# Optimization experiments

Hardware: AMD Instinct MI355X
Metric: run time of the kernel (lower is better)

## Reference

```python
import jax, jax.numpy as jnp
import numpy as np
import math

B, S, D, H = 2, 2048, 1024, 16
D_K = D // H


def setup_inputs() -> dict:
    key = jax.random.key(0)
    ks = jax.random.split(key, 9)
    scale = 0.02
    return {
        "query": jax.random.normal(ks[0], (B, S, D), dtype=jnp.float32),
        "key": jax.random.normal(ks[1], (B, S, D), dtype=jnp.float32),
        "value": jax.random.normal(ks[2], (B, S, D), dtype=jnp.float32),
        "padding_mask": jax.random.bernoulli(ks[3], 0.1, (B, 1, 1, S)),
        "Wq": jax.random.normal(ks[4], (D, D), dtype=jnp.float32) * scale,
        "bq": jnp.zeros((D,), dtype=jnp.float32),
        "Wk": jax.random.normal(ks[5], (D, D), dtype=jnp.float32) * scale,
        "bk": jnp.zeros((D,), dtype=jnp.float32),
        "Wv": jax.random.normal(ks[6], (D, D), dtype=jnp.float32) * scale,
        "bv": jnp.zeros((D,), dtype=jnp.float32),
        "Wo": jax.random.normal(ks[7], (D, D), dtype=jnp.float32) * scale,
        "bo": jnp.zeros((D,), dtype=jnp.float32),
    }


def reference(query, key, value, padding_mask, Wq, bq, Wk, bk, Wv, bv, Wo, bo):
    # projections -> [B, H, S, d_k]
    q = (query @ Wq + bq).reshape(B, S, H, D_K).transpose(0, 2, 1, 3)
    k = (key @ Wk + bk).reshape(B, S, H, D_K).transpose(0, 2, 1, 3)
    v = (value @ Wv + bv).reshape(B, S, H, D_K).transpose(0, 2, 1, 3)

    # scores: [B, H, S, S]
    scores = jnp.einsum("bhqd,bhkd->bhqk", q, k) / math.sqrt(D_K)

    # faithful to original: triu(scores, 1).bool() -> True where upper-tri score != 0,
    # masked positions get value 1e-10 (NOT -inf) before softmax
    causal_mask = jnp.triu(scores, k=1) != 0
    scores = jnp.where(causal_mask, jnp.float32(1e-10), scores)
    scores = jnp.where(padding_mask, jnp.float32(1e-10), scores)

    attn = jax.nn.softmax(scores, axis=-1)
    out = jnp.einsum("bhqk,bhkd->bhqd", attn, v)  # [B, H, S, d_k]
    out = out.transpose(0, 2, 1, 3).reshape(B, S, D)
    return out @ Wo + bo
```

## Files before the change

### kernel.cpp

```cpp
#include <hip/hip_runtime.h>
#include <hip/hip_bf16.h>
#include <cstdint>
#include <cstddef>

typedef __hip_bfloat16 bf16;
typedef __attribute__((ext_vector_type(8))) short short8;
typedef __attribute__((ext_vector_type(4))) short s4v;
typedef __attribute__((ext_vector_type(4))) float floatx4;

#define B_ 2
#define S_ 2048
#define D_ 1024
#define H_ 16
#define DK_ 64
#define M_ 4096
#define HEADELEMS 131072
#define TILEELEMS 4096
#define QSCALE 0.1803368801111204f

struct __align__(8) bf16x4 { bf16 x, y, z, w; };

__device__ __forceinline__ floatx4 mfma16(short8 a, short8 b, floatx4 c) {
  return __builtin_amdgcn_mfma_f32_16x16x32_bf16(a, b, c, 0, 0, 0);
}
__device__ __forceinline__ void gl_lds16(const bf16* g, bf16* l) {
  __builtin_amdgcn_global_load_lds((const __attribute__((address_space(1))) void*)g,
                                   (__attribute__((address_space(3))) void*)l, 16, 0, 0);
}
__device__ __forceinline__ float bs2f(short s) {
  bf16 b = *reinterpret_cast<bf16*>(&s);
  return __bfloat162float(b);
}
__device__ __forceinline__ s4v pack4(float p0, float p1, float p2, float p3) {
  union { __hip_bfloat162 h; short2 s; } ua, ub;
  ua.h = __float22bfloat162_rn(make_float2(p0, p1));
  ub.h = __float22bfloat162_rn(make_float2(p2, p3));
  s4v r = {ua.s.x, ua.s.y, ub.s.x, ub.s.y};
  return r;
}
__device__ __forceinline__ float fast_exp2(float x) {
#if __has_builtin(__builtin_amdgcn_exp2f)
  return __builtin_amdgcn_exp2f(x);
#else
  float r; asm("v_exp_f32 %0, %1" : "=v"(r) : "v"(x)); return r;
#endif
}

__global__ void prep_kernel(const float* __restrict__ q_in, const float* __restrict__ k_in,
                            const float* __restrict__ v_in,
                            const float* __restrict__ Wq, const float* __restrict__ Wk,
                            const float* __restrict__ Wv, const float* __restrict__ Wo,
                            bf16* __restrict__ xq, bf16* __restrict__ xk, bf16* __restrict__ xv,
                            bf16* __restrict__ wqt, bf16* __restrict__ wkt,
                            bf16* __restrict__ wvt, bf16* __restrict__ wot,
                            const unsigned int* __restrict__ pmask, int* __restrict__ flag) {
  __shared__ bf16 tile[64][66];
  __shared__ int sbyte;
  const int blk = blockIdx.x;
  const int tid = threadIdx.x;
  if (blk < 12288) {
    const int z = blk >> 12;
    const int i = ((blk & 4095) << 8) | tid;
    const float* src = (z == 0) ? q_in : (z == 1) ? k_in : v_in;
    bf16* dst = (z == 0) ? xq : (z == 1) ? xk : xv;
    float4 v = ((const float4*)src)[i];
    bf16x4 o = { __float2bfloat16(v.x), __float2bfloat16(v.y),
                 __float2bfloat16(v.z), __float2bfloat16(v.w) };
    ((bf16x4*)dst)[i] = o;
  } else if (blk < 13312) {
    const int t = blk - 12288;
    const int z = t >> 8;
    const int rc = t & 255;
    const int r0 = (rc >> 4) * 64, c0 = (rc & 15) * 64;
    const float* src = (z == 0) ? Wq : (z == 1) ? Wk : (z == 2) ? Wv : Wo;
    bf16* dst = (z == 0) ? wqt : (z == 1) ? wkt : (z == 2) ? wvt : wot;
    const int lr = tid >> 4;
    const int lc4 = (tid & 15) * 4;
#pragma unroll
    for (int i = 0; i < 4; ++i) {
      const int r = lr + i * 16;
      float4 v = *(const float4*)(src + (size_t)(r0 + r) * D_ + c0 + lc4);
      tile[r][lc4 + 0] = __float2bfloat16(v.x);
      tile[r][lc4 + 1] = __float2bfloat16(v.y);
      tile[r][lc4 + 2] = __float2bfloat16(v.z);
      tile[r][lc4 + 3] = __float2bfloat16(v.w);
    }
    __syncthreads();
    const int orr = tid & 63;
    const int oc0 = tid >> 6;
#pragma unroll
    for (int j = 0; j < 16; ++j) {
      const int oc = oc0 + j * 4;
      dst[(size_t)(c0 + oc) * D_ + r0 + orr] = tile[orr][oc];
    }
  } else {
    if (tid == 0) sbyte = 0;
    __syncthreads();
    for (int i = tid; i < (B_ * S_) / 4; i += 256) {
      const unsigned int v = pmask[i];
      if (((v & 0xFEFEFEFEu) == 0u) && ((v & 0xFFFFFF00u) != 0u)) sbyte = 1;
    }
    __syncthreads();
    if (tid == 0) *flag = sbyte;
  }
}

template<int MT>
__global__ __launch_bounds__(256, 2) void gemm_k(
    const bf16* __restrict__ A0, const bf16* __restrict__ A1, const bf16* __restrict__ A2,
    const bf16* __restrict__ W0, const bf16* __restrict__ W1, const bf16* __restrict__ W2,
    const float* __restrict__ b0, const float* __restrict__ b1, const float* __restrict__ b2,
    void* __restrict__ O0, void* __restrict__ O1, void* __restrict__ O2,
    const int mode01, const int Kd, const float sc)
{
  constexpr int ROWS = MT + 128;
  __shared__ __align__(16) bf16 sh[2 * ROWS * 64];
  const int z = blockIdx.z;
  const bf16* A = (z == 0) ? A0 : (z == 1) ? A1 : A2;
  const bf16* W = (z == 0) ? W0 : (z == 1) ? W1 : W2;
  const float* bias = (z == 0) ? b0 : (z == 1) ? b1 : b2;
  void* Cout = (z == 0) ? O0 : (z == 1) ? O1 : O2;
  const int mode = (z == 2) ? 1 : mode01;
  const float scz = (z == 0) ? sc : 1.f;

  constexpr int MI = MT / 32;
  const int tid = threadIdx.x;
  const int wave = tid >> 6, lane = tid & 63;
  const int quad = lane >> 4, lc = lane & 15;
  const int wm = (wave >> 1) * (MT / 2), wn = (wave & 1) * 64;
  const int m0 = blockIdx.x * MT, n0 = blockIdx.y * 128;

  const floatx4 zero4 = {0.f, 0.f, 0.f, 0.f};
  floatx4 acc[MI][4];
#pragma unroll
  for (int mi = 0; mi < MI; ++mi)
#pragma unroll
    for (int ni = 0; ni < 4; ++ni) acc[mi][ni] = zero4;

  const int srow = lane >> 3;
  const int schunk = ((lane & 7) ^ srow) * 8;
  const bf16* Ag = A + (size_t)(m0 + wave * (MT / 4) + srow) * Kd + schunk;
  const bf16* Bg = W + (size_t)(n0 + wave * 32 + srow) * Kd + schunk;

  auto stage = [&](bf16* buf, int k0) {
    bf16* As0 = buf + wave * (MT / 4) * 64;
    bf16* Bs0 = buf + MT * 64 + wave * 32 * 64;
#pragma unroll
    for (int j = 0; j < MT / 32; ++j)
      gl_lds16(Ag + k0 + (size_t)(j * 8) * Kd, As0 + j * 512);
#pragma unroll
    for (int j = 0; j < 4; ++j)
      gl_lds16(Bg + k0 + (size_t)(j * 8) * Kd, Bs0 + j * 512);
  };

  stage(sh, 0);
  asm volatile("s_waitcnt vmcnt(0)" ::: "memory");
  __syncthreads();

  int cur = 0;
  for (int k0 = 0; k0 < Kd; k0 += 64) {
    bf16* cbuf = cur ? sh + ROWS * 64 : sh;
    bf16* nbuf = cur ? sh : sh + ROWS * 64;
    const bool more = (k0 + 64 < Kd);
    if (more) stage(nbuf, k0 + 64);

    const bf16* Ar = cbuf;
    const bf16* Br = cbuf + MT * 64;
    short8 af[2][MI], bfr[2][4];
#pragma unroll
    for (int kk = 0; kk < 2; ++kk) {
#pragma unroll
      for (int i = 0; i < MI; ++i)
        af[kk][i] = *(const short8*)(Ar + (wm + i * 16 + lc) * 64
                                     + (((kk * 4 + quad) ^ (lc & 7)) * 8));
#pragma unroll
      for (int i = 0; i < 4; ++i)
        bfr[kk][i] = *(const short8*)(Br + (wn + i * 16 + lc) * 64
                                      + (((kk * 4 + quad) ^ (lc & 7)) * 8));
    }
#pragma unroll
    for (int kk = 0; kk < 2; ++kk)
#pragma unroll
      for (int mi = 0; mi < MI; ++mi)
#pragma unroll
        for (int ni = 0; ni < 4; ++ni)
          acc[mi][ni] = mfma16(af[kk][mi], bfr[kk][ni], acc[mi][ni]);

    __syncthreads();
    cur ^= 1;
  }

  if (mode == 2) {
    float* out = (float*)Cout;
#pragma unroll
    for (int mi = 0; mi < MI; ++mi)
#pragma unroll
      for (int ni = 0; ni < 4; ++ni) {
        const int col = n0 + wn + ni * 16 + lc;
        const float bv = bias[col];
        const int rbase = m0 + wm + mi * 16 + quad * 4;
#pragma unroll
        for (int r = 0; r < 4; ++r)
          out[(size_t)(rbase + r) * D_ + col] = acc[mi][ni][r] + bv;
      }
  } else {
    bf16* pool = sh + wave * 2048;
    float bvs[4];
#pragma unroll
    for (int ni = 0; ni < 4; ++ni) bvs[ni] = bias[n0 + wn + ni * 16 + lc];
    const int hcol = (n0 + wn) >> 6;
    const int mglob = m0 + wm;
    bf16* outb = (bf16*)Cout + (size_t)((mglob >> 11) * H_ + hcol) * HEADELEMS
               + (size_t)((mglob & (S_ - 1)) >> 6) * TILEELEMS;
#pragma unroll
    for (int half = 0; half < MI / 2; ++half) {
#pragma unroll
      for (int mi2 = 0; mi2 < 2; ++mi2) {
        const int mi = half * 2 + mi2;
#pragma unroll
        for (int ni = 0; ni < 4; ++ni) {
          const int dkl = ni * 16 + lc;
#pragma unroll
          for (int r = 0; r < 4; ++r) {
            const float v = (acc[mi][ni][r] + bvs[ni]) * scz;
            int idx;
            if (mode == 0) {
              const int c = (mi2 * 2 + (dkl >> 5)) * 64 + ((dkl >> 3) & 3) * 16 + quad * 4 + r;
              idx = c * 8 + (dkl & 7);
            } else {
              const int c = (mi2 * 4 + (dkl >> 4)) * 64 + quad * 16 + (dkl & 15);
              idx = c * 4 + r;
            }
            pool[idx] = __float2bfloat16(v);
          }
        }
      }
#pragma unroll
      for (int t = 0; t < 4; ++t) {
        const short8 vv = *(const short8*)(pool + t * 512 + lane * 8);
        *(short8*)(outb + half * 2048 + t * 512 + lane * 8) = vv;
      }
    }
  }
}

__global__ void suf_kernel(const bf16* __restrict__ vp, float* __restrict__ suf) {
  __shared__ float ts[32 * 64];
  const int bhid = blockIdx.x;
  const bf16* vb = vp + (size_t)bhid * HEADELEMS;
  const int tid = threadIdx.x;
  const int dk = tid & 63, g = tid >> 6;
  const int dkt = dk >> 4, lck = dk & 15;
  for (int T = g * 8; T < g * 8 + 8; ++T) {
    float sum = 0.f;
#pragma unroll
    for (int w = 0; w < 4; ++w)
#pragma unroll
      for (int qd = 0; qd < 4; ++qd) {
        const s4v x = *(const s4v*)(vb + (size_t)T * TILEELEMS
                                    + (size_t)(((w * 4 + dkt) * 64 + qd * 16 + lck)) * 4);
        sum += bs2f(x[0]) + bs2f(x[1]) + bs2f(x[2]) + bs2f(x[3]);
      }
    ts[T * 64 + dk] = sum;
  }
  __syncthreads();
  if (g == 0) {
    float run = 0.f;
    float* out = suf + (size_t)bhid * (33 * 64);
    out[32 * 64 + dk] = 0.f;
    for (int T = 31; T >= 0; --T) { run += ts[T * 64 + dk]; out[T * 64 + dk] = run; }
  }
}

template<bool DIAGP>
__device__ __forceinline__ void qk_tile(const short8 ak0, const short8 ak1,
                                        const short8 (&qf)[4][2],
                                        const unsigned int (&pmb)[4], const int T,
                                        short8 (&pB)[4], const int half,
                                        const int w, const int quad, const int lc,
                                        const bool diag) {
  const floatx4 z4 = {0.f, 0.f, 0.f, 0.f};
  const short ONE = (short)0x3F80;
  bool mm[4];
#pragma unroll
  for (int r = 0; r < 4; ++r) mm[r] = ((pmb[r] >> T) & 1u) != 0u;
#pragma unroll
  for (int qt = 0; qt < 4; ++qt) {
    if (DIAGP && diag && w > qt) {
      s4v o1 = {ONE, ONE, ONE, ONE};
      ((s4v*)&pB[qt])[half] = o1;
      continue;
    }
    floatx4 s = mfma16(ak0, qf[qt][0], z4);
    s = mfma16(ak1, qf[qt][1], s);
    float pv[4];
#pragma unroll
    for (int r = 0; r < 4; ++r) {
      bool m = mm[r];
      if (DIAGP && diag && w == qt) m = m || (quad * 4 + r > lc);
      pv[r] = m ? 1.f : fast_exp2(s[r]);
    }
    ((s4v*)&pB[qt])[half] = pack4(pv[0], pv[1], pv[2], pv[3]);
  }
}

__device__ __forceinline__ void pv_step(const short8 (&av)[4], const short8 (&pB)[4],
                                        const short8 ones, floatx4 (&lsum)[4],
                                        floatx4 (&oacc)[4][4]) {
#pragma unroll
  for (int qt = 0; qt < 4; ++qt) lsum[qt] = mfma16(ones, pB[qt], lsum[qt]);
#pragma unroll
  for (int dkt = 0; dkt < 4; ++dkt)
#pragma unroll
    for (int qt = 0; qt < 4; ++qt)
      oacc[dkt][qt] = mfma16(av[dkt], pB[qt], oacc[dkt][qt]);
}

__device__ __forceinline__ void stage8(const bf16* kb, const bf16* vb, bf16* slot,
                                       const int T0, const int T1,
                                       const int wl, const int wreg) {
  const bf16* k0 = kb + (size_t)T0 * TILEELEMS + wl;
  const bf16* k1 = kb + (size_t)T1 * TILEELEMS + wl;
  const bf16* v0 = vb + (size_t)T0 * TILEELEMS + wl;
  const bf16* v1 = vb + (size_t)T1 * TILEELEMS + wl;
  gl_lds16(k0,       slot + wreg);
  gl_lds16(k0 + 512, slot + wreg + 512);
  gl_lds16(k1,       slot + 4096 + wreg);
  gl_lds16(k1 + 512, slot + 4096 + wreg + 512);
  gl_lds16(v0,       slot + 8192 + wreg);
  gl_lds16(v0 + 512, slot + 8192 + wreg + 512);
  gl_lds16(v1,       slot + 12288 + wreg);
  gl_lds16(v1 + 512, slot + 12288 + wreg + 512);
}

__global__ __launch_bounds__(256, 2) void attn_kernel(
    const bf16* __restrict__ qp, const bf16* __restrict__ kp,
    const bf16* __restrict__ vp, const float* __restrict__ suf,
    const void* __restrict__ pad, const int* __restrict__ flag,
    bf16* __restrict__ oa)
{
  __shared__ __align__(16) bf16 lds[32768];

  const int lin = blockIdx.x;
  const int xcd = lin & 7;
  const int t = lin >> 3;
  const int grp = t >> 4;
  const int jq = t & 15;
  const int bh = xcd + 8 * grp;
  const int b = bh >> 4, h = bh & 15;

  const int tid = threadIdx.x;
  const int w = tid >> 6, lane = tid & 63, quad = lane >> 4, lc = lane & 15;
  const int bytemode = *flag;

  const int wreg = w * 1024;
  const int wl = wreg + lane * 8;
  const int vl = wreg + lane * 4;

  const bf16* kb = kp + (size_t)bh * HEADELEMS;
  const bf16* vb = vp + (size_t)bh * HEADELEMS;

  const short ONE = (short)0x3F80;
  const short8 ones = {ONE, ONE, ONE, ONE, ONE, ONE, ONE, ONE};

  unsigned int pmb[4] = {0u, 0u, 0u, 0u};
  if (bytemode) {
    const unsigned char* pp = (const unsigned char*)pad + b * S_ + w * 16 + quad * 4;
#pragma unroll
    for (int T = 0; T < 32; ++T) {
      const uchar4 u = *(const uchar4*)(pp + T * 64);
      pmb[0] |= (u.x ? 1u : 0u) << T;
      pmb[1] |= (u.y ? 1u : 0u) << T;
      pmb[2] |= (u.z ? 1u : 0u) << T;
      pmb[3] |= (u.w ? 1u : 0u) << T;
    }
  } else {
    const int* pp = (const int*)pad + b * S_ + w * 16 + quad * 4;
#pragma unroll
    for (int T = 0; T < 32; ++T) {
      const int4 u = *(const int4*)(pp + (size_t)T * 64);
      pmb[0] |= (u.x ? 1u : 0u) << T;
      pmb[1] |= (u.y ? 1u : 0u) << T;
      pmb[2] |= (u.z ? 1u : 0u) << T;
      pmb[3] |= (u.w ? 1u : 0u) << T;
    }
  }

#pragma unroll 1
  for (int qsel = 0; qsel < 2; ++qsel) {
    const int myqt = qsel ? jq : 31 - jq;
    const int mynt = myqt + 1;
    const int np = (mynt + 1) >> 1;

    const bf16* qb = qp + (size_t)bh * HEADELEMS + (size_t)myqt * TILEELEMS;
    gl_lds16(qb + wl,       lds + 16384 + wreg);
    gl_lds16(qb + wl + 512, lds + 16384 + wreg + 512);
    stage8(kb, vb, lds, 0, 1, wl, wreg);
    asm volatile("s_waitcnt vmcnt(0)" ::: "memory");
    __syncthreads();

    short8 qf[4][2];
#pragma unroll
    for (int qt = 0; qt < 4; ++qt)
#pragma unroll
      for (int hh = 0; hh < 2; ++hh)
        qf[qt][hh] = *(const short8*)(lds + 16384 + qt * 1024 + hh * 512 + lane * 8);
    __syncthreads();

    const floatx4 zero4 = {0.f, 0.f, 0.f, 0.f};
    floatx4 oacc[4][4];
#pragma unroll
    for (int i = 0; i < 4; ++i)
#pragma unroll
      for (int jj = 0; jj < 4; ++jj) oacc[i][jj] = zero4;
    floatx4 lsum[4] = {zero4, zero4, zero4, zero4};

#pragma unroll 1
    for (int p = 0; p < np; ++p) {
      const bool more = (p + 1 < np);
      if (more) {
        stage8(kb, vb, lds + (((p + 1) & 1) << 14), 2 * p + 2, 2 * p + 3, wl, wreg);
        asm volatile("s_waitcnt vmcnt(12)" ::: "memory");
      } else {
        asm volatile("s_waitcnt vmcnt(4)" ::: "memory");
      }
      __builtin_amdgcn_sched_barrier(0);

      bf16* slot = lds + ((p & 1) << 14);
      const short8 ak00 = *(const short8*)(slot + wl);
      const short8 ak01 = *(const short8*)(slot + wl + 512);
      const short8 ak10 = *(const short8*)(slot + 4096 + wl);
      const short8 ak11 = *(const short8*)(slot + 4096 + wl + 512);

      const int T0 = 2 * p, T1 = 2 * p + 1;
      short8 pB[4];
      if (more) {
        qk_tile<false>(ak00, ak01, qf, pmb, T0, pB, 0, w, quad, lc, false);
        qk_tile<false>(ak10, ak11, qf, pmb, T1, pB, 1, w, quad, lc, false);
      } else {
        qk_tile<true>(ak00, ak01, qf, pmb, T0, pB, 0, w, quad, lc, T0 == mynt - 1);
        if (T1 < mynt) {
          qk_tile<true>(ak10, ak11, qf, pmb, T1, pB, 1, w, quad, lc, true);
        } else {
          const s4v zz = {0, 0, 0, 0};
#pragma unroll
          for (int qt = 0; qt < 4; ++qt) ((s4v*)&pB[qt])[1] = zz;
        }
      }

      if (more) asm volatile("s_waitcnt vmcnt(8)" ::: "memory");
      else      asm volatile("s_waitcnt vmcnt(0)" ::: "memory");
      __builtin_amdgcn_sched_barrier(0);

      short8 av[4];
#pragma unroll
      for (int dkt = 0; dkt < 4; ++dkt) {
        ((s4v*)&av[dkt])[0] = *(const s4v*)(slot + 8192 + vl + dkt * 256);
        ((s4v*)&av[dkt])[1] = *(const s4v*)(slot + 12288 + vl + dkt * 256);
      }
      pv_step(av, pB, ones, lsum, oacc);
    }

    __syncthreads();

    float* fbuf = (float*)lds;
    bf16* obuf = lds + 8704;
    float* lbuf = (float*)(lds + 13312);

#pragma unroll
    for (int qt = 0; qt < 4; ++qt)
      if (quad == 0) lbuf[w * 64 + qt * 16 + lc] = lsum[qt][0];
    __syncthreads();
    float ls = lbuf[0 * 64 + w * 16 + lc] + lbuf[1 * 64 + w * 16 + lc]
             + lbuf[2 * 64 + w * 16 + lc] + lbuf[3 * 64 + w * 16 + lc];
    ls += (float)(S_ - mynt * 64);
    const float linv = 1.f / ls;
    const float* sufp = suf + (size_t)bh * (33 * 64) + mynt * 64;

#pragma unroll
    for (int dktG = 0; dktG < 4; ++dktG) {
#pragma unroll
      for (int qt = 0; qt < 4; ++qt) {
        const floatx4 a = oacc[dktG][qt];
        float* dst = fbuf + (w * 4 + qt) * 272 + lc;
#pragma unroll
        for (int r = 0; r < 4; ++r) dst[(quad * 4 + r) * 17] = a[r];
      }
      __syncthreads();
      const float4 sv4 = *(const float4*)(sufp + dktG * 16 + quad * 4);
      float v[4];
#pragma unroll
      for (int r = 0; r < 4; ++r) {
        const int e = (quad * 4 + r) * 17 + lc;
        v[r] = fbuf[(0 * 4 + w) * 272 + e] + fbuf[(1 * 4 + w) * 272 + e]
             + fbuf[(2 * 4 + w) * 272 + e] + fbuf[(3 * 4 + w) * 272 + e];
      }
      v[0] = (v[0] + sv4.x) * linv; v[1] = (v[1] + sv4.y) * linv;
      v[2] = (v[2] + sv4.z) * linv; v[3] = (v[3] + sv4.w) * linv;
      bf16x4 pk = { __float2bfloat16(v[0]), __float2bfloat16(v[1]),
                    __float2bfloat16(v[2]), __float2bfloat16(v[3]) };
      *(bf16x4*)(obuf + (w * 16 + lc) * 72 + dktG * 16 + quad * 4) = pk;
      __syncthreads();
    }

    const size_t obase = (size_t)(b * S_ + myqt * 64) * D_ + h * 64;
#pragma unroll
    for (int it = 0; it < 2; ++it) {
      const int idx = it * 256 + tid;
      const int row = idx >> 3, c8 = (idx & 7) * 8;
      const short8 vv = *(const short8*)(obuf + row * 72 + c8);
      *(short8*)(oa + obase + (size_t)row * D_ + c8) = vv;
    }
    __syncthreads();
  }
}

extern "C" void kernel_launch(void* const* d_in, const int* in_sizes, int n_in,
                              void* d_out, int out_size, void* d_ws, size_t ws_size,
                              hipStream_t stream) {
  (void)in_sizes; (void)n_in; (void)out_size; (void)ws_size;
  const float* q_in = (const float*)d_in[0];
  const float* k_in = (const float*)d_in[1];
  const float* v_in = (const float*)d_in[2];
  const void*  pmask = d_in[3];
  const float* Wq = (const float*)d_in[4];
  const float* bq = (const float*)d_in[5];
  const float* Wk = (const float*)d_in[6];
  const float* bk = (const float*)d_in[7];
  const float* Wv = (const float*)d_in[8];
  const float* bv = (const float*)d_in[9];
  const float* Wo = (const float*)d_in[10];
  const float* bo = (const float*)d_in[11];

  char* ws = (char*)d_ws;
  bf16* xq  = (bf16*)(ws + 0);
  bf16* xk  = (bf16*)(ws + 8388608);
  bf16* xv  = (bf16*)(ws + 16777216);
  bf16* wqt = (bf16*)(ws + 25165824);
  bf16* wkt = (bf16*)(ws + 27262976);
  bf16* wvt = (bf16*)(ws + 29360128);
  bf16* wot = (bf16*)(ws + 31457280);
  bf16* qpp = (bf16*)(ws + 33554432);
  bf16* kpp = (bf16*)(ws + 41943040);
  bf16* vpp = (bf16*)(ws + 50331648);
  float* suf = (float*)(ws + 25165824);
  int*  flg = (int*)(ws + 58720256);
  bf16* oa  = xq;

  prep_kernel<<<13313, 256, 0, stream>>>(q_in, k_in, v_in, Wq, Wk, Wv, Wo,
                                         xq, xk, xv, wqt, wkt, wvt, wot,
                                         (const unsigned int*)pmask, flg);

  gemm_k<128><<<dim3(32, 8, 3), 256, 0, stream>>>(xq, xk, xv, wqt, wkt, wvt,
                                                  bq, bk, bv, qpp, kpp, vpp, 0, D_, QSCALE);
  suf_kernel<<<32, 256, 0, stream>>>(vpp, suf);

  attn_kernel<<<512, 256, 0, stream>>>(qpp, kpp, vpp, suf, pmask, flg, oa);

  gemm_k<128><<<dim3(32, 8, 1), 256, 0, stream>>>(oa, oa, oa, wot, wot, wot,
                                                  bo, bo, bo, d_out, d_out, d_out, 2, D_, 1.f);
}
```

Baseline: 221.4 us.

## Split attention to one query tile per block with single-buffered per-wave LDS

Each attention block now handles a single query tile instead of a balanced pair, so 1024 blocks are launched. A rotated index mapping spreads the short and long causal tiles evenly across blocks. LDS is halved by dropping the double buffer: each wave reads its own K/V slice into registers, then immediately issues the next global-to-LDS loads into the same slots. Together with launch bounds of 4 blocks per CU, the aim is to raise occupancy and let other waves hide load latency. The cost is less prefetch overlap inside a single wave and more per-block prologue and epilogue overhead.

```diff
diff --git a/kernel.cpp b/kernel.cpp
--- a/kernel.cpp
+++ b/kernel.cpp
@@ -19,6 +19,7 @@
 #define QSCALE 0.1803368801111204f
 
 struct __align__(8) bf16x4 { bf16 x, y, z, w; };
+struct __align__(4) bf16x2 { bf16 x, y; };
 
 __device__ __forceinline__ floatx4 mfma16(short8 a, short8 b, floatx4 c) {
   return __builtin_amdgcn_mfma_f32_16x16x32_bf16(a, b, c, 0, 0, 0);
@@ -213,10 +214,10 @@
     bf16* outb = (bf16*)Cout + (size_t)((mglob >> 11) * H_ + hcol) * HEADELEMS
                + (size_t)((mglob & (S_ - 1)) >> 6) * TILEELEMS;
 #pragma unroll
-    for (int half = 0; half < MI / 2; ++half) {
+    for (int half2 = 0; half2 < MI / 2; ++half2) {
 #pragma unroll
       for (int mi2 = 0; mi2 < 2; ++mi2) {
-        const int mi = half * 2 + mi2;
+        const int mi = half2 * 2 + mi2;
 #pragma unroll
         for (int ni = 0; ni < 4; ++ni) {
           const int dkl = ni * 16 + lc;
@@ -238,7 +239,7 @@
 #pragma unroll
       for (int t = 0; t < 4; ++t) {
         const short8 vv = *(const short8*)(pool + t * 512 + lane * 8);
-        *(short8*)(outb + half * 2048 + t * 512 + lane * 8) = vv;
+        *(short8*)(outb + half2 * 2048 + t * 512 + lane * 8) = vv;
       }
     }
   }
@@ -304,50 +305,25 @@
   }
 }
 
-__device__ __forceinline__ void pv_step(const short8 (&av)[4], const short8 (&pB)[4],
-                                        const short8 ones, floatx4 (&lsum)[4],
-                                        floatx4 (&oacc)[4][4]) {
-#pragma unroll
-  for (int qt = 0; qt < 4; ++qt) lsum[qt] = mfma16(ones, pB[qt], lsum[qt]);
-#pragma unroll
-  for (int dkt = 0; dkt < 4; ++dkt)
-#pragma unroll
-    for (int qt = 0; qt < 4; ++qt)
-      oacc[dkt][qt] = mfma16(av[dkt], pB[qt], oacc[dkt][qt]);
-}
-
-__device__ __forceinline__ void stage8(const bf16* kb, const bf16* vb, bf16* slot,
-                                       const int T0, const int T1,
-                                       const int wl, const int wreg) {
-  const bf16* k0 = kb + (size_t)T0 * TILEELEMS + wl;
-  const bf16* k1 = kb + (size_t)T1 * TILEELEMS + wl;
-  const bf16* v0 = vb + (size_t)T0 * TILEELEMS + wl;
-  const bf16* v1 = vb + (size_t)T1 * TILEELEMS + wl;
-  gl_lds16(k0,       slot + wreg);
-  gl_lds16(k0 + 512, slot + wreg + 512);
-  gl_lds16(k1,       slot + 4096 + wreg);
-  gl_lds16(k1 + 512, slot + 4096 + wreg + 512);
-  gl_lds16(v0,       slot + 8192 + wreg);
-  gl_lds16(v0 + 512, slot + 8192 + wreg + 512);
-  gl_lds16(v1,       slot + 12288 + wreg);
-  gl_lds16(v1 + 512, slot + 12288 + wreg + 512);
-}
-
-__global__ __launch_bounds__(256, 2) void attn_kernel(
+__global__ __launch_bounds__(256, 4) void attn_kernel(
     const bf16* __restrict__ qp, const bf16* __restrict__ kp,
     const bf16* __restrict__ vp, const float* __restrict__ suf,
     const void* __restrict__ pad, const int* __restrict__ flag,
     bf16* __restrict__ oa)
 {
-  __shared__ __align__(16) bf16 lds[32768];
+  __shared__ __align__(16) bf16 lds[16384];
 
   const int lin = blockIdx.x;
   const int xcd = lin & 7;
-  const int t = lin >> 3;
-  const int grp = t >> 4;
-  const int jq = t & 15;
+  const int i2 = lin >> 3;
+  const int grp = i2 >> 5;
+  const int r5 = i2 & 31;
   const int bh = xcd + 8 * grp;
+  const int rr = (grp & 2) ? ((r5 + 16) & 31) : r5;
+  const int myqt = (grp & 1) ? rr : (31 - rr);
   const int b = bh >> 4, h = bh & 15;
+  const int mynt = myqt + 1;
+  const int np = (mynt + 1) >> 1;
 
   const int tid = threadIdx.x;
   const int w = tid >> 6, lane = tid & 63, quad = lane >> 4, lc = lane & 15;
@@ -386,132 +362,152 @@
     }
   }
 
+  const bf16* qb = qp + (size_t)bh * HEADELEMS + (size_t)myqt * TILEELEMS;
+  gl_lds16(qb + wl,       lds + 8192 + wreg);
+  gl_lds16(qb + wl + 512, lds + 8192 + wreg + 512);
+  gl_lds16(kb + wl,       lds + wreg);
+  gl_lds16(kb + wl + 512, lds + wreg + 512);
+  gl_lds16(vb + wl,       lds + 4096 + wreg);
+  gl_lds16(vb + wl + 512, lds + 4096 + wreg + 512);
+  gl_lds16(vb + TILEELEMS + wl,       lds + 12288 + wreg);
+  gl_lds16(vb + TILEELEMS + wl + 512, lds + 12288 + wreg + 512);
+  asm volatile("s_waitcnt vmcnt(6)" ::: "memory");
+  __builtin_amdgcn_s_barrier();
+  __builtin_amdgcn_sched_barrier(0);
+
+  short8 qf[4][2];
+#pragma unroll
+  for (int qt = 0; qt < 4; ++qt)
+#pragma unroll
+    for (int hh = 0; hh < 2; ++hh)
+      qf[qt][hh] = *(const short8*)(lds + 8192 + qt * 1024 + hh * 512 + lane * 8);
+  asm volatile("s_waitcnt lgkmcnt(0)" ::: "memory");
+  __builtin_amdgcn_sched_barrier(0);
+  __builtin_amdgcn_s_barrier();
+  gl_lds16(kb + TILEELEMS + wl,       lds + 8192 + wreg);
+  gl_lds16(kb + TILEELEMS + wl + 512, lds + 8192 + wreg + 512);
+
+  const floatx4 zero4 = {0.f, 0.f, 0.f, 0.f};
+  floatx4 oacc[4][4];
+#pragma unroll
+  for (int i = 0; i < 4; ++i)
+#pragma unroll
+    for (int jj = 0; jj < 4; ++jj) oacc[i][jj] = zero4;
+  floatx4 lsum[4] = {zero4, zero4, zero4, zero4};
+
 #pragma unroll 1
-  for (int qsel = 0; qsel < 2; ++qsel) {
-    const int myqt = qsel ? jq : 31 - jq;
-    const int mynt = myqt + 1;
-    const int np = (mynt + 1) >> 1;
-
-    const bf16* qb = qp + (size_t)bh * HEADELEMS + (size_t)myqt * TILEELEMS;
-    gl_lds16(qb + wl,       lds + 16384 + wreg);
-    gl_lds16(qb + wl + 512, lds + 16384 + wreg + 512);
-    stage8(kb, vb, lds, 0, 1, wl, wreg);
+  for (int p = 0; p < np; ++p) {
     asm volatile("s_waitcnt vmcnt(0)" ::: "memory");
+    __builtin_amdgcn_sched_barrier(0);
+
+    const short8 ak00 = *(const short8*)(lds + wl);
+    const short8 ak01 = *(const short8*)(lds + wl + 512);
+    const short8 ak10 = *(const short8*)(lds + 8192 + wl);
+    const short8 ak11 = *(const short8*)(lds + 8192 + wl + 512);
+    s4v va0[4], va1[4];
+#pragma unroll
+    for (int dkt = 0; dkt < 4; ++dkt) {
+      va0[dkt] = *(const s4v*)(lds + 4096 + vl + dkt * 256);
+      va1[dkt] = *(const s4v*)(lds + 12288 + vl + dkt * 256);
+    }
+    asm volatile("s_waitcnt lgkmcnt(0)" ::: "memory");
+    __builtin_amdgcn_sched_barrier(0);
+
+    if (p + 1 < np) {
+      const bf16* k2 = kb + (size_t)(2 * p + 2) * TILEELEMS + wl;
+      const bf16* v2 = vb + (size_t)(2 * p + 2) * TILEELEMS + wl;
+      gl_lds16(k2,       lds + wreg);
+      gl_lds16(k2 + 512, lds + wreg + 512);
+      gl_lds16(v2,       lds + 4096 + wreg);
+      gl_lds16(v2 + 512, lds + 4096 + wreg + 512);
+      const bf16* k3 = k2 + TILEELEMS;
+      const bf16* v3 = v2 + TILEELEMS;
+      gl_lds16(k3,       lds + 8192 + wreg);
+      gl_lds16(k3 + 512, lds + 8192 + wreg + 512);
+      gl_lds16(v3,       lds + 12288 + wreg);
+      gl_lds16(v3 + 512, lds + 12288 + wreg + 512);
+    }
+
+    const int T0 = 2 * p, T1 = 2 * p + 1;
+    short8 pB[4];
+    if (p + 1 < np) {
+      qk_tile<false>(ak00, ak01, qf, pmb, T0, pB, 0, w, quad, lc, false);
+      qk_tile<false>(ak10, ak11, qf, pmb, T1, pB, 1, w, quad, lc, false);
+    } else {
+      qk_tile<true>(ak00, ak01, qf, pmb, T0, pB, 0, w, quad, lc, T0 == mynt - 1);
+      if (T1 < mynt) {
+        qk_tile<true>(ak10, ak11, qf, pmb, T1, pB, 1, w, quad, lc, true);
+      } else {
+        const s4v zz = {0, 0, 0, 0};
+#pragma unroll
+        for (int qt = 0; qt < 4; ++qt) ((s4v*)&pB[qt])[1] = zz;
+      }
+    }
+
+    short8 av[4];
+#pragma unroll
+    for (int dkt = 0; dkt < 4; ++dkt) {
+      ((s4v*)&av[dkt])[0] = va0[dkt];
+      ((s4v*)&av[dkt])[1] = va1[dkt];
+    }
+#pragma unroll
+    for (int qt = 0; qt < 4; ++qt) lsum[qt] = mfma16(ones, pB[qt], lsum[qt]);
+#pragma unroll
+    for (int dkt = 0; dkt < 4; ++dkt)
+#pragma unroll
+      for (int qt = 0; qt < 4; ++qt)
+        oacc[dkt][qt] = mfma16(av[dkt], pB[qt], oacc[dkt][qt]);
+  }
+
+  __syncthreads();
+
+  float* fbuf = (float*)lds;
+  bf16* obuf = lds + 8704;
+  float* lbuf = (float*)(lds + 13312);
+
+#pragma unroll
+  for (int qt = 0; qt < 4; ++qt)
+    if (quad == 0) lbuf[w * 64 + qt * 16 + lc] = lsum[qt][0];
+  __syncthreads();
+  float ls = lbuf[0 * 64 + w * 16 + lc] + lbuf[1 * 64 + w * 16 + lc]
+           + lbuf[2 * 64 + w * 16 + lc] + lbuf[3 * 64 + w * 16 + lc];
+  ls += (float)(S_ - mynt * 64);
+  const float linv = 1.f / ls;
+  const float* sufp = suf + (size_t)bh * (33 * 64) + mynt * 64;
+
+#pragma unroll
+  for (int dktG = 0; dktG < 4; ++dktG) {
+#pragma unroll
+    for (int qt = 0; qt < 4; ++qt) {
+      const floatx4 a = oacc[dktG][qt];
+      float* dst = fbuf + (w * 4 + qt) * 272 + lc;
+#pragma unroll
+      for (int r = 0; r < 4; ++r) dst[(quad * 4 + r) * 17] = a[r];
+    }
     __syncthreads();
-
-    short8 qf[4][2];
-#pragma unroll
-    for (int qt = 0; qt < 4; ++qt)
-#pragma unroll
-      for (int hh = 0; hh < 2; ++hh)
-        qf[qt][hh] = *(const short8*)(lds + 16384 + qt * 1024 + hh * 512 + lane * 8);
+    const float4 sv4 = *(const float4*)(sufp + dktG * 16 + quad * 4);
+    float v[4];
+#pragma unroll
+    for (int r = 0; r < 4; ++r) {
+      const int e = (quad * 4 + r) * 17 + lc;
+      v[r] = fbuf[(0 * 4 + w) * 272 + e] + fbuf[(1 * 4 + w) * 272 + e]
+           + fbuf[(2 * 4 + w) * 272 + e] + fbuf[(3 * 4 + w) * 272 + e];
+    }
+    v[0] = (v[0] + sv4.x) * linv; v[1] = (v[1] + sv4.y) * linv;
+    v[2] = (v[2] + sv4.z) * linv; v[3] = (v[3] + sv4.w) * linv;
+    bf16x4 pk = { __float2bfloat16(v[0]), __float2bfloat16(v[1]),
+                  __float2bfloat16(v[2]), __float2bfloat16(v[3]) };
+    *(bf16x4*)(obuf + (w * 16 + lc) * 72 + dktG * 16 + quad * 4) = pk;
     __syncthreads();
-
-    const floatx4 zero4 = {0.f, 0.f, 0.f, 0.f};
-    floatx4 oacc[4][4];
-#pragma unroll
-    for (int i = 0; i < 4; ++i)
-#pragma unroll
-      for (int jj = 0; jj < 4; ++jj) oacc[i][jj] = zero4;
-    floatx4 lsum[4] = {zero4, zero4, zero4, zero4};
-
-#pragma unroll 1
-    for (int p = 0; p < np; ++p) {
-      const bool more = (p + 1 < np);
-      if (more) {
-        stage8(kb, vb, lds + (((p + 1) & 1) << 14), 2 * p + 2, 2 * p + 3, wl, wreg);
-        asm volatile("s_waitcnt vmcnt(12)" ::: "memory");
-      } else {
-        asm volatile("s_waitcnt vmcnt(4)" ::: "memory");
-      }
-      __builtin_amdgcn_sched_barrier(0);
-
-      bf16* slot = lds + ((p & 1) << 14);
-      const short8 ak00 = *(const short8*)(slot + wl);
-      const short8 ak01 = *(const short8*)(slot + wl + 512);
-      const short8 ak10 = *(const short8*)(slot + 4096 + wl);
-      const short8 ak11 = *(const short8*)(slot + 4096 + wl + 512);
-
-      const int T0 = 2 * p, T1 = 2 * p + 1;
-      short8 pB[4];
-      if (more) {
-        qk_tile<false>(ak00, ak01, qf, pmb, T0, pB, 0, w, quad, lc, false);
-        qk_tile<false>(ak10, ak11, qf, pmb, T1, pB, 1, w, quad, lc, false);
-      } else {
-        qk_tile<true>(ak00, ak01, qf, pmb, T0, pB, 0, w, quad, lc, T0 == mynt - 1);
-        if (T1 < mynt) {
-          qk_tile<true>(ak10, ak11, qf, pmb, T1, pB, 1, w, quad, lc, true);
-        } else {
-          const s4v zz = {0, 0, 0, 0};
-#pragma unroll
-          for (int qt = 0; qt < 4; ++qt) ((s4v*)&pB[qt])[1] = zz;
-        }
-      }
-
-      if (more) asm volatile("s_waitcnt vmcnt(8)" ::: "memory");
-      else      asm volatile("s_waitcnt vmcnt(0)" ::: "memory");
-      __builtin_amdgcn_sched_barrier(0);
-
-      short8 av[4];
-#pragma unroll
-      for (int dkt = 0; dkt < 4; ++dkt) {
-        ((s4v*)&av[dkt])[0] = *(const s4v*)(slot + 8192 + vl + dkt * 256);
-        ((s4v*)&av[dkt])[1] = *(const s4v*)(slot + 12288 + vl + dkt * 256);
-      }
-      pv_step(av, pB, ones, lsum, oacc);
-    }
-
-    __syncthreads();
-
-    float* fbuf = (float*)lds;
-    bf16* obuf = lds + 8704;
-    float* lbuf = (float*)(lds + 13312);
-
-#pragma unroll
-    for (int qt = 0; qt < 4; ++qt)
-      if (quad == 0) lbuf[w * 64 + qt * 16 + lc] = lsum[qt][0];
-    __syncthreads();
-    float ls = lbuf[0 * 64 + w * 16 + lc] + lbuf[1 * 64 + w * 16 + lc]
-             + lbuf[2 * 64 + w * 16 + lc] + lbuf[3 * 64 + w * 16 + lc];
-    ls += (float)(S_ - mynt * 64);
-    const float linv = 1.f / ls;
-    const float* sufp = suf + (size_t)bh * (33 * 64) + mynt * 64;
-
-#pragma unroll
-    for (int dktG = 0; dktG < 4; ++dktG) {
-#pragma unroll
-      for (int qt = 0; qt < 4; ++qt) {
-        const floatx4 a = oacc[dktG][qt];
-        float* dst = fbuf + (w * 4 + qt) * 272 + lc;
-#pragma unroll
-        for (int r = 0; r < 4; ++r) dst[(quad * 4 + r) * 17] = a[r];
-      }
-      __syncthreads();
-      const float4 sv4 = *(const float4*)(sufp + dktG * 16 + quad * 4);
-      float v[4];
-#pragma unroll
-      for (int r = 0; r < 4; ++r) {
-        const int e = (quad * 4 + r) * 17 + lc;
-        v[r] = fbuf[(0 * 4 + w) * 272 + e] + fbuf[(1 * 4 + w) * 272 + e]
-             + fbuf[(2 * 4 + w) * 272 + e] + fbuf[(3 * 4 + w) * 272 + e];
-      }
-      v[0] = (v[0] + sv4.x) * linv; v[1] = (v[1] + sv4.y) * linv;
-      v[2] = (v[2] + sv4.z) * linv; v[3] = (v[3] + sv4.w) * linv;
-      bf16x4 pk = { __float2bfloat16(v[0]), __float2bfloat16(v[1]),
-                    __float2bfloat16(v[2]), __float2bfloat16(v[3]) };
-      *(bf16x4*)(obuf + (w * 16 + lc) * 72 + dktG * 16 + quad * 4) = pk;
-      __syncthreads();
-    }
-
-    const size_t obase = (size_t)(b * S_ + myqt * 64) * D_ + h * 64;
-#pragma unroll
-    for (int it = 0; it < 2; ++it) {
-      const int idx = it * 256 + tid;
-      const int row = idx >> 3, c8 = (idx & 7) * 8;
-      const short8 vv = *(const short8*)(obuf + row * 72 + c8);
-      *(short8*)(oa + obase + (size_t)row * D_ + c8) = vv;
-    }
-    __syncthreads();
+  }
+
+  const size_t obase = (size_t)(b * S_ + myqt * 64) * D_ + h * 64;
+#pragma unroll
+  for (int it = 0; it < 2; ++it) {
+    const int idx = it * 256 + tid;
+    const int row = idx >> 3, c8 = (idx & 7) * 8;
+    const short8 vv = *(const short8*)(obuf + row * 72 + c8);
+    *(short8*)(oa + obase + (size_t)row * D_ + c8) = vv;
   }
 }
 
@@ -555,7 +551,7 @@
                                                   bq, bk, bv, qpp, kpp, vpp, 0, D_, QSCALE);
   suf_kernel<<<32, 256, 0, stream>>>(vpp, suf);
 
-  attn_kernel<<<512, 256, 0, stream>>>(qpp, kpp, vpp, suf, pmask, flg, oa);
+  attn_kernel<<<1024, 256, 0, stream>>>(qpp, kpp, vpp, suf, pmask, flg, oa);
 
   gemm_k<128><<<dim3(32, 8, 1), 256, 0, stream>>>(oa, oa, oa, wot, wot, wot,
                                                   bo, bo, bo, d_out, d_out, d_out, 2, D_, 1.f);
```

New measurement: 392.7 us. +77.4%, slower.
